# Kernel optimization log

Hardware: AMD Instinct MI355X
Metric: run time of the kernel (lower is better)

## Reference

```python
import jax, jax.numpy as jnp
import numpy as np
from jax import lax

BAD = -10000.0
K = 10
W = 512  # window_size


def setup_inputs() -> dict:
    key = jax.random.key(0)
    k1, k2, k3, k4 = jax.random.split(key, 4)
    S, B, P, D, R = 4, 256, 32768, 256, 1000
    return {
        "relation": jax.random.randint(k1, (S, B), 0, R, dtype=jnp.int32),
        "head": jax.random.randint(k2, (S, B), 0, P, dtype=jnp.int32),
        "entity_embedding": jax.random.normal(k3, (S, P, D), dtype=jnp.float32),
        "relation_embedding": jax.random.normal(k4, (R, D), dtype=jnp.float32),
    }


def reference(relation, head, entity_embedding, relation_embedding):
    S, B = relation.shape
    P, D = entity_embedding.shape[1], entity_embedding.shape[2]
    Q = S * B            # total queries after all_gather
    NBEST = K + 1
    n_rep = -(-P // W)   # ceil

    # all_gather of queries across shards (every shard sees all queries)
    rel_all = relation.reshape(-1)                                   # (Q,)
    head_emb_all = entity_embedding[jnp.arange(S)[:, None], head]    # (S,B,D)
    head_emb_all = head_emb_all.reshape(Q, D)
    # DistMult score_tails: <h, r, t> ; fold h*r into one query vector
    qvec = head_emb_all * relation_embedding[rel_all]                # (Q,D)

    init_sc = jnp.full((S, Q, NBEST), BAD, dtype=jnp.float32)
    init_ix = jnp.full((S, Q, NBEST), P, dtype=jnp.int32)

    def step(carry, w):
        sc, ix = carry
        start = w * W
        # local idx of this window, clamped like the torch mask branch
        raw = start + jnp.arange(W, dtype=jnp.int32)                 # (W,)
        valid = raw < P
        slide = jnp.where(valid, raw, P - 1)
        neg = lax.dynamic_slice_in_dim(entity_embedding,
                                       jnp.minimum(start, P - W), W, axis=1)  # (S,W,D)
        scores_w = jnp.einsum('qd,swd->sqw', qvec, neg)              # (S,Q,W)
        scores_w = scores_w + BAD * (~valid).astype(scores_w.dtype)
        all_sc = jnp.concatenate([scores_w, sc], axis=-1)            # (S,Q,W+NBEST)
        all_ix = jnp.concatenate(
            [jnp.broadcast_to(slide, (S, Q, W)), ix], axis=-1)
        top_sc, top_pos = lax.top_k(all_sc, NBEST)
        top_ix = jnp.take_along_axis(all_ix, top_pos, axis=-1)
        return (top_sc, top_ix), None

    (best_sc, best_ix), _ = lax.scan(step, (init_sc, init_ix),
                                     jnp.arange(n_rep, dtype=jnp.int32))

    # all_to_all: (src_shard, dst_shard, bs, nbest) -> (dst, src, bs, nbest)
    best_sc = best_sc.reshape(S, S, B, NBEST).transpose(1, 0, 2, 3)
    best_ix = best_ix.reshape(S, S, B, NBEST).transpose(1, 0, 2, 3)

    # mask out placeholder / padding local indices (shard_counts == P)
    best_sc = best_sc + BAD * (best_ix >= P).astype(best_sc.dtype)

    # shard_and_idx_to_entity: interleaved global ids, padded column for idx==P
    base = jnp.arange(P, dtype=jnp.int32)[None, :] * S \
        + jnp.arange(S, dtype=jnp.int32)[:, None]                    # (S,P)
    table = jnp.concatenate(
        [base, jnp.full((S, 1), -1, dtype=jnp.int32)], axis=1)       # (S,P+1)
    src = jnp.arange(S, dtype=jnp.int32)[None, :, None, None]
    best_gid = table[src, best_ix]                                   # (S,S,B,NBEST)

    # per destination shard: merge the S per-source-shard top-(k+1) lists
    sc_flat = best_sc.transpose(0, 2, 1, 3).reshape(S, B, S * NBEST)
    gid_flat = best_gid.transpose(0, 2, 1, 3).reshape(S, B, S * NBEST)
    topk_sc, topk_pos = lax.top_k(sc_flat, K)                        # (S,B,K)
    topk_gid = jnp.take_along_axis(gid_flat, topk_pos, axis=-1)
    return topk_gid, topk_sc
```

## Files before the change

### kernel.cpp

```cpp
#include <hip/hip_runtime.h>

#define SS 4
#define BB 256
#define PP 32768
#define DD 256
#define QQ 1024
#define NN 131072
#define KTOP 10
#define QTILE 128
#define WQ 32
#define NCHUNK 64
#define CHROWS 2048
#define PANEL 64
#define NPANEL (CHROWS / PANEL)
#define JCH 8
#define MSLOT 20
#define ROWG 33
#define ROWE (ROWG * 8)
#define PANB (PANEL * ROWG * 16)
#define KEYMASK 0xFFFFF800u
#define MWS 132
#define CVB 4096

typedef __attribute__((ext_vector_type(8))) short bf16x8;
typedef __attribute__((ext_vector_type(4))) short s16x4;
typedef __attribute__((ext_vector_type(4))) float f32x4;
typedef __attribute__((ext_vector_type(16))) float f32x16;
typedef __attribute__((ext_vector_type(4))) unsigned int u32x4;

static __device__ __forceinline__ short f2bf(float f) {
    union { float f; unsigned u; } v; v.f = f;
    unsigned r = (v.u + 0x7FFFu + ((v.u >> 16) & 1u)) >> 16;
    return (short)r;
}
static __device__ __forceinline__ unsigned umax(unsigned a, unsigned b) { return a > b ? a : b; }
static __device__ __forceinline__ unsigned umin(unsigned a, unsigned b) { return a < b ? a : b; }
static __device__ __forceinline__ unsigned med3u(unsigned k, unsigned a, unsigned b) {
    unsigned d;
    asm("v_med3_u32 %0, %1, %2, %3" : "=v"(d) : "v"(k), "v"(a), "v"(b));
    return d;
}

__global__ void prep_kernel(const int* __restrict__ rel, const int* __restrict__ head,
                            const float* __restrict__ E, const float* __restrict__ R,
                            short* __restrict__ Ebf, short* __restrict__ qbf) {
    if (blockIdx.x < CVB) {
        size_t base = (size_t)blockIdx.x * 8192;
        #pragma unroll
        for (int c = 0; c < 8; c++) {
            size_t idx = base + (size_t)c * 1024 + (size_t)threadIdx.x * 4;
            f32x4 a = *(const f32x4*)(E + idx);
            s16x4 o;
            o[0] = f2bf(a[0]); o[1] = f2bf(a[1]); o[2] = f2bf(a[2]); o[3] = f2bf(a[3]);
            *(s16x4*)(Ebf + idx) = o;
        }
    } else {
        int q = blockIdx.x - CVB, d = threadIdx.x;
        int s1 = q >> 8;
        float f = E[((size_t)(s1 * PP + head[q])) * DD + d] * R[(size_t)rel[q] * DD + d];
        qbf[q * DD + d] = f2bf(f);
    }
}

__launch_bounds__(256, 2)
__global__ void score_topk_kernel(const short* __restrict__ Ebf, const short* __restrict__ qbf,
                                  unsigned* __restrict__ parts) {
    __shared__ __align__(16) char smem[2 * PANB];

    const int tid  = threadIdx.x;
    const int wave = tid >> 6;
    const int lane = tid & 63;
    const int lh   = lane >> 5;
    const int ln   = lane & 31;
    const int mtile = blockIdx.x >> 6;
    const int chunk = blockIdx.x & 63;

    short* const buf0 = (short*)smem;
    short* const buf1 = (short*)(smem + PANB);

    bf16x8 afrag[16];
    {
        const int arow = mtile * QTILE + wave * WQ + ln;
        #pragma unroll
        for (int ks = 0; ks < 16; ks++)
            afrag[ks] = *(const bf16x8*)(qbf + arow * DD + ks * 16 + lh * 8);
    }

    unsigned lst[16][4];
    #pragma unroll
    for (int r = 0; r < 16; r++)
        #pragma unroll
        for (int i = 0; i < 4; i++) lst[r][i] = 0u;

    const int n0c = chunk * CHROWS;

    const int srow = tid >> 5, sslot = tid & 31;
    const int goff = srow * DD + sslot * 8;
    const int loff = srow * ROWE + sslot * 8;

    const short* const rb0a = buf0 + ln * ROWE + lh * 8;
    const short* const rb0b = rb0a + 32 * ROWE;
    const short* const rb1a = buf1 + ln * ROWE + lh * 8;
    const short* const rb1b = rb1a + 32 * ROWE;

    bf16x8 st[8];

    {
        const short* pp = Ebf + (size_t)n0c * DD;
        #pragma unroll
        for (int it = 0; it < 8; it++)
            st[it] = *(const bf16x8*)(pp + goff + it * 2048);
        #pragma unroll
        for (int it = 0; it < 8; it++)
            *(bf16x8*)(buf0 + loff + it * (8 * ROWE)) = st[it];
    }

    #define PREFETCH(pnext)                                                        \
        {                                                                          \
            const short* pp = Ebf + (size_t)(n0c + (pnext) * PANEL) * DD;          \
            _Pragma("unroll")                                                      \
            for (int it = 0; it < 8; it++)                                         \
                st[it] = *(const bf16x8*)(pp + goff + it * 2048);                  \
        }
    #define STORE_TO(bufp)                                                         \
        {                                                                          \
            _Pragma("unroll")                                                      \
            for (int it = 0; it < 8; it++)                                         \
                *(bf16x8*)((bufp) + loff + it * (8 * ROWE)) = st[it];              \
        }
    #define COMPUTE(ra, rb, pcur)                                                  \
        {                                                                          \
            f32x16 acc0, acc1;                                                     \
            _Pragma("unroll")                                                      \
            for (int r = 0; r < 16; r++) { acc0[r] = 256.0f; acc1[r] = 256.0f; }   \
            _Pragma("unroll")                                                      \
            for (int ks = 0; ks < 16; ks++) {                                      \
                bf16x8 x0 = *(const bf16x8*)((ra) + ks * 16);                      \
                bf16x8 x1 = *(const bf16x8*)((rb) + ks * 16);                      \
                acc0 = __builtin_amdgcn_mfma_f32_32x32x16_bf16(afrag[ks], x0, acc0, 0, 0, 0); \
                acc1 = __builtin_amdgcn_mfma_f32_32x32x16_bf16(afrag[ks], x1, acc1, 0, 0, 0); \
            }                                                                      \
            const unsigned c0 = (unsigned)((pcur) * 64 + ln);                      \
            const unsigned c1 = c0 + 32u;                                          \
            _Pragma("unroll")                                                      \
            for (int r = 0; r < 16; r++) {                                         \
                unsigned key = (__float_as_uint(acc0[r]) & KEYMASK) | c0;          \
                unsigned n0 = med3u(key, lst[r][0], lst[r][1]);                    \
                unsigned n1 = med3u(key, lst[r][1], lst[r][2]);                    \
                unsigned n2 = med3u(key, lst[r][2], lst[r][3]);                    \
                lst[r][3] = umax(key, lst[r][3]);                                  \
                lst[r][0] = n0; lst[r][1] = n1; lst[r][2] = n2;                    \
            }                                                                      \
            _Pragma("unroll")                                                      \
            for (int r = 0; r < 16; r++) {                                         \
                unsigned key = (__float_as_uint(acc1[r]) & KEYMASK) | c1;          \
                unsigned n0 = med3u(key, lst[r][0], lst[r][1]);                    \
                unsigned n1 = med3u(key, lst[r][1], lst[r][2]);                    \
                unsigned n2 = med3u(key, lst[r][2], lst[r][3]);                    \
                lst[r][3] = umax(key, lst[r][3]);                                  \
                lst[r][0] = n0; lst[r][1] = n1; lst[r][2] = n2;                    \
            }                                                                      \
        }

    for (int p = 0; p < NPANEL; p += 2) {
        __syncthreads();
        PREFETCH(p + 1);
        COMPUTE(rb0a, rb0b, p);
        STORE_TO(buf1);
        __syncthreads();
        if (p + 2 < NPANEL) PREFETCH(p + 2);
        COMPUTE(rb1a, rb1b, p + 1);
        if (p + 2 < NPANEL) STORE_TO(buf0);
    }

    #undef PREFETCH
    #undef STORE_TO
    #undef COMPUTE

    __syncthreads();
    unsigned* mw = (unsigned*)smem + (size_t)wave * (WQ * MWS);
    #pragma unroll
    for (int r = 0; r < 16; r++) {
        int q = (r & 3) + 8 * (r >> 2) + 4 * lh;
        u32x4 v; v[0] = lst[r][0]; v[1] = lst[r][1]; v[2] = lst[r][2]; v[3] = lst[r][3];
        *(u32x4*)(mw + q * MWS + ln * 4) = v;
    }
    if (lane < 32) {
        unsigned rr[JCH];
        #pragma unroll
        for (int i = 0; i < JCH; i++) rr[i] = 0u;
        #pragma unroll
        for (int j = 0; j < 32; j++) {
            u32x4 v = *(const u32x4*)(mw + lane * MWS + j * 4);
            #pragma unroll
            for (int e = 0; e < 4; e++) {
                unsigned x = v[e];
                unsigned t0 = med3u(x, rr[0], rr[1]);
                unsigned t1 = med3u(x, rr[1], rr[2]);
                unsigned t2 = med3u(x, rr[2], rr[3]);
                unsigned t3 = med3u(x, rr[3], rr[4]);
                unsigned t4 = med3u(x, rr[4], rr[5]);
                unsigned t5 = med3u(x, rr[5], rr[6]);
                unsigned t6 = med3u(x, rr[6], rr[7]);
                rr[7] = umax(x, rr[7]);
                rr[0]=t0; rr[1]=t1; rr[2]=t2; rr[3]=t3; rr[4]=t4; rr[5]=t5; rr[6]=t6;
            }
        }
        const int qg = mtile * QTILE + wave * WQ + lane;
        unsigned* dst = parts + ((size_t)qg * NCHUNK + chunk) * JCH;
        #pragma unroll
        for (int i = 0; i < JCH; i++) dst[i] = rr[JCH - 1 - i];
    }
}

__global__ void finalize_kernel(const int* __restrict__ rel, const int* __restrict__ head,
                                const float* __restrict__ E, const float* __restrict__ R,
                                const unsigned* __restrict__ parts, float* __restrict__ out) {
    __shared__ float qv[DD];
    __shared__ int   gl[MSLOT];
    __shared__ float rsc[MSLOT];
    __shared__ int   rgid[MSLOT];

    const int q = blockIdx.x;
    const int tid = threadIdx.x;
    const int wave = tid >> 6, lane = tid & 63;
    const int s1 = q >> 8;

    qv[tid] = E[((size_t)(s1 * PP + head[q])) * DD + tid] * R[(size_t)rel[q] * DD + tid];

    if (wave == 0) {
        unsigned run[JCH];
        const unsigned* src = parts + ((size_t)q * NCHUNK + lane) * JCH;
        #pragma unroll
        for (int j = 0; j < JCH; j++) run[j] = src[j];
        for (int r = 0; r < MSLOT; r++) {
            unsigned best = run[0]; int bl = lane;
            #pragma unroll
            for (int off = 32; off >= 1; off >>= 1) {
                unsigned ob = __shfl_xor(best, off);
                int ol = __shfl_xor(bl, off);
                if (ob > best || (ob == best && ol < bl)) { best = ob; bl = ol; }
            }
            if (lane == bl) {
                int col = (int)(best & 0x7FFu);
                int n = lane * CHROWS + col;
                gl[r] = ((n & (PP - 1)) << 2) | (n >> 15);
                #pragma unroll
                for (int j = 0; j < JCH - 1; j++) run[j] = run[j + 1];
                run[JCH - 1] = 0u;
            }
        }
    }
    __syncthreads();

    f32x4 qq = *(const f32x4*)(qv + lane * 4);
    #pragma unroll
    for (int c = 0; c < MSLOT / 4; c++) {
        int j = wave * (MSLOT / 4) + c;
        int gid = gl[j];
        int n = (gid & 3) * PP + (gid >> 2);
        f32x4 ev = *(const f32x4*)(E + (size_t)n * DD + lane * 4);
        f32x4 p = qq * ev;
        float s = (p[0] + p[1]) + (p[2] + p[3]);
        #pragma unroll
        for (int off = 32; off >= 1; off >>= 1) s += __shfl_xor(s, off);
        if (lane == 0) { rsc[j] = s; rgid[j] = gid; }
    }
    __syncthreads();

    if (tid < 64) {
        float a = (tid < MSLOT) ? rsc[tid] : -1e30f;
        int   g = (tid < MSLOT) ? rgid[tid] : 0;
        for (int r = 0; r < KTOP; r++) {
            float ps = a; int pg = g; int plm = tid;
            #pragma unroll
            for (int off = 32; off >= 1; off >>= 1) {
                float os = __shfl_xor(ps, off);
                int   og = __shfl_xor(pg, off);
                int   ol = __shfl_xor(plm, off);
                if (os > ps || (os == ps && ol < plm)) { ps = os; pg = og; plm = ol; }
            }
            if (tid == 0) {
                out[q * KTOP + r]             = (float)pg;
                out[QQ * KTOP + q * KTOP + r] = ps;
            }
            if (tid == plm) a = -1e30f;
        }
    }
}

extern "C" void kernel_launch(void* const* d_in, const int* in_sizes, int n_in,
                              void* d_out, int out_size, void* d_ws, size_t ws_size,
                              hipStream_t stream) {
    const int*   rel  = (const int*)d_in[0];
    const int*   head = (const int*)d_in[1];
    const float* E    = (const float*)d_in[2];
    const float* R    = (const float*)d_in[3];

    char* ws = (char*)d_ws;
    short* Ebf = (short*)ws;
    short* qbf = (short*)(ws + (size_t)NN * DD * 2);
    unsigned* parts = (unsigned*)(ws + (size_t)NN * DD * 2 + (size_t)QQ * DD * 2);

    prep_kernel<<<dim3(CVB + QQ), dim3(256), 0, stream>>>(rel, head, E, R, Ebf, qbf);
    score_topk_kernel<<<dim3((QQ / QTILE) * NCHUNK), dim3(256), 0, stream>>>(Ebf, qbf, parts);
    finalize_kernel<<<dim3(QQ), dim3(256), 0, stream>>>(rel, head, E, R, parts, (float*)d_out);
}
```

Measured before the change: 307.6 us.

## Stage panels via direct global-to-LDS loads with XOR swizzle and software-pipelined top-k

```diff
diff --git a/kernel.cpp b/kernel.cpp
--- a/kernel.cpp
+++ b/kernel.cpp
@@ -15,11 +15,9 @@
 #define NPANEL (CHROWS / PANEL)
 #define JCH 8
 #define MSLOT 20
-#define ROWG 33
-#define ROWE (ROWG * 8)
-#define PANB (PANEL * ROWG * 16)
+#define PANB (PANEL * DD * 2)
 #define KEYMASK 0xFFFFF800u
-#define MWS 132
+#define MWS 128
 #define CVB 4096
 
 typedef __attribute__((ext_vector_type(8))) short bf16x8;
@@ -34,7 +32,6 @@
     return (short)r;
 }
 static __device__ __forceinline__ unsigned umax(unsigned a, unsigned b) { return a > b ? a : b; }
-static __device__ __forceinline__ unsigned umin(unsigned a, unsigned b) { return a < b ? a : b; }
 static __device__ __forceinline__ unsigned med3u(unsigned k, unsigned a, unsigned b) {
     unsigned d;
     asm("v_med3_u32 %0, %1, %2, %3" : "=v"(d) : "v"(k), "v"(a), "v"(b));
@@ -74,9 +71,7 @@
     const int ln   = lane & 31;
     const int mtile = blockIdx.x >> 6;
     const int chunk = blockIdx.x & 63;
-
-    short* const buf0 = (short*)smem;
-    short* const buf1 = (short*)(smem + PANB);
+    const int wavu = __builtin_amdgcn_readfirstlane(tid) >> 6;
 
     bf16x8 afrag[16];
     {
@@ -92,98 +87,91 @@
         #pragma unroll
         for (int i = 0; i < 4; i++) lst[r][i] = 0u;
 
-    const int n0c = chunk * CHROWS;
-
-    const int srow = tid >> 5, sslot = tid & 31;
-    const int goff = srow * DD + sslot * 8;
-    const int loff = srow * ROWE + sslot * 8;
-
-    const short* const rb0a = buf0 + ln * ROWE + lh * 8;
-    const short* const rb0b = rb0a + 32 * ROWE;
-    const short* const rb1a = buf1 + ln * ROWE + lh * 8;
-    const short* const rb1b = rb1a + 32 * ROWE;
-
-    bf16x8 st[8];
-
-    {
-        const short* pp = Ebf + (size_t)n0c * DD;
-        #pragma unroll
-        for (int it = 0; it < 8; it++)
-            st[it] = *(const bf16x8*)(pp + goff + it * 2048);
-        #pragma unroll
-        for (int it = 0; it < 8; it++)
-            *(bf16x8*)(buf0 + loff + it * (8 * ROWE)) = st[it];
-    }
-
-    #define PREFETCH(pnext)                                                        \
-        {                                                                          \
-            const short* pp = Ebf + (size_t)(n0c + (pnext) * PANEL) * DD;          \
-            _Pragma("unroll")                                                      \
-            for (int it = 0; it < 8; it++)                                         \
-                st[it] = *(const bf16x8*)(pp + goff + it * 2048);                  \
-        }
-    #define STORE_TO(bufp)                                                         \
-        {                                                                          \
-            _Pragma("unroll")                                                      \
-            for (int it = 0; it < 8; it++)                                         \
-                *(bf16x8*)((bufp) + loff + it * (8 * ROWE)) = st[it];              \
-        }
-    #define COMPUTE(ra, rb, pcur)                                                  \
-        {                                                                          \
-            f32x16 acc0, acc1;                                                     \
-            _Pragma("unroll")                                                      \
-            for (int r = 0; r < 16; r++) { acc0[r] = 256.0f; acc1[r] = 256.0f; }   \
-            _Pragma("unroll")                                                      \
-            for (int ks = 0; ks < 16; ks++) {                                      \
-                bf16x8 x0 = *(const bf16x8*)((ra) + ks * 16);                      \
-                bf16x8 x1 = *(const bf16x8*)((rb) + ks * 16);                      \
-                acc0 = __builtin_amdgcn_mfma_f32_32x32x16_bf16(afrag[ks], x0, acc0, 0, 0, 0); \
-                acc1 = __builtin_amdgcn_mfma_f32_32x32x16_bf16(afrag[ks], x1, acc1, 0, 0, 0); \
-            }                                                                      \
-            const unsigned c0 = (unsigned)((pcur) * 64 + ln);                      \
-            const unsigned c1 = c0 + 32u;                                          \
-            _Pragma("unroll")                                                      \
-            for (int r = 0; r < 16; r++) {                                         \
-                unsigned key = (__float_as_uint(acc0[r]) & KEYMASK) | c0;          \
-                unsigned n0 = med3u(key, lst[r][0], lst[r][1]);                    \
-                unsigned n1 = med3u(key, lst[r][1], lst[r][2]);                    \
-                unsigned n2 = med3u(key, lst[r][2], lst[r][3]);                    \
-                lst[r][3] = umax(key, lst[r][3]);                                  \
-                lst[r][0] = n0; lst[r][1] = n1; lst[r][2] = n2;                    \
-            }                                                                      \
-            _Pragma("unroll")                                                      \
-            for (int r = 0; r < 16; r++) {                                         \
-                unsigned key = (__float_as_uint(acc1[r]) & KEYMASK) | c1;          \
-                unsigned n0 = med3u(key, lst[r][0], lst[r][1]);                    \
-                unsigned n1 = med3u(key, lst[r][1], lst[r][2]);                    \
-                unsigned n2 = med3u(key, lst[r][2], lst[r][3]);                    \
-                lst[r][3] = umax(key, lst[r][3]);                                  \
-                lst[r][0] = n0; lst[r][1] = n1; lst[r][2] = n2;                    \
-            }                                                                      \
-        }
+    int addrk[16];
+    #pragma unroll
+    for (int ks = 0; ks < 16; ks++)
+        addrk[ks] = ln * 512 + ((((ks << 1) | lh) ^ (ln & 7)) << 4);
+
+    int soff[8];
+    #pragma unroll
+    for (int it = 0; it < 8; it++) {
+        int row = (((wavu * 8 + it) << 1) | lh);
+        soff[it] = row * 512 + ((ln ^ (row & 7)) << 4);
+    }
+
+    const char* const pb = (const char*)(Ebf + (size_t)(chunk * CHROWS) * DD);
+
+    #define STAGE(POFF, LOFF)                                                          \
+        {                                                                              \
+            _Pragma("unroll")                                                          \
+            for (int it = 0; it < 8; it++)                                             \
+                __builtin_amdgcn_global_load_lds(                                      \
+                    (const __attribute__((address_space(1))) void*)(pb + (POFF) + soff[it]), \
+                    (__attribute__((address_space(3))) void*)(smem + (LOFF) + (wavu * 8 + it) * 1024), \
+                    16, 0, 0);                                                         \
+        }
+
+    #define MFMA_PANEL(A0, A1, LOFF)                                                   \
+        {                                                                              \
+            _Pragma("unroll")                                                          \
+            for (int r = 0; r < 16; r++) { A0[r] = 256.0f; A1[r] = 256.0f; }           \
+            _Pragma("unroll")                                                          \
+            for (int ks = 0; ks < 16; ks++) {                                          \
+                bf16x8 x0 = *(const bf16x8*)(smem + addrk[ks] + (LOFF));               \
+                bf16x8 x1 = *(const bf16x8*)(smem + addrk[ks] + (LOFF) + 16384);       \
+                A0 = __builtin_amdgcn_mfma_f32_32x32x16_bf16(afrag[ks], x0, A0, 0, 0, 0); \
+                A1 = __builtin_amdgcn_mfma_f32_32x32x16_bf16(afrag[ks], x1, A1, 0, 0, 0); \
+            }                                                                          \
+        }
+
+    #define KEYS(A0, A1, PIDX)                                                         \
+        {                                                                              \
+            const unsigned c0k = (unsigned)((PIDX) * 64 + ln);                         \
+            const unsigned c1k = c0k + 32u;                                            \
+            _Pragma("unroll")                                                          \
+            for (int r = 0; r < 16; r++) {                                             \
+                unsigned key = (__float_as_uint(A0[r]) & KEYMASK) | c0k;               \
+                unsigned n0 = med3u(key, lst[r][0], lst[r][1]);                        \
+                unsigned n1 = med3u(key, lst[r][1], lst[r][2]);                        \
+                unsigned n2 = med3u(key, lst[r][2], lst[r][3]);                        \
+                lst[r][3] = umax(key, lst[r][3]);                                      \
+                lst[r][0] = n0; lst[r][1] = n1; lst[r][2] = n2;                        \
+                key = (__float_as_uint(A1[r]) & KEYMASK) | c1k;                        \
+                n0 = med3u(key, lst[r][0], lst[r][1]);                                 \
+                n1 = med3u(key, lst[r][1], lst[r][2]);                                 \
+                n2 = med3u(key, lst[r][2], lst[r][3]);                                 \
+                lst[r][3] = umax(key, lst[r][3]);                                      \
+                lst[r][0] = n0; lst[r][1] = n1; lst[r][2] = n2;                        \
+            }                                                                          \
+        }
+
+    f32x16 accA0, accA1, accB0, accB1;
+
+    STAGE(0, 0);
+    __syncthreads();
 
     for (int p = 0; p < NPANEL; p += 2) {
+        STAGE((p + 1) * PANB, PANB);
+        MFMA_PANEL(accA0, accA1, 0);
+        if (p > 0) KEYS(accB0, accB1, p - 1);
         __syncthreads();
-        PREFETCH(p + 1);
-        COMPUTE(rb0a, rb0b, p);
-        STORE_TO(buf1);
+        if (p + 2 < NPANEL) STAGE((p + 2) * PANB, 0);
+        MFMA_PANEL(accB0, accB1, PANB);
+        KEYS(accA0, accA1, p);
         __syncthreads();
-        if (p + 2 < NPANEL) PREFETCH(p + 2);
-        COMPUTE(rb1a, rb1b, p + 1);
-        if (p + 2 < NPANEL) STORE_TO(buf0);
-    }
-
-    #undef PREFETCH
-    #undef STORE_TO
-    #undef COMPUTE
-
-    __syncthreads();
+    }
+    KEYS(accB0, accB1, NPANEL - 1);
+
+    #undef STAGE
+    #undef MFMA_PANEL
+    #undef KEYS
+
     unsigned* mw = (unsigned*)smem + (size_t)wave * (WQ * MWS);
     #pragma unroll
     for (int r = 0; r < 16; r++) {
         int q = (r & 3) + 8 * (r >> 2) + 4 * lh;
         u32x4 v; v[0] = lst[r][0]; v[1] = lst[r][1]; v[2] = lst[r][2]; v[3] = lst[r][3];
-        *(u32x4*)(mw + q * MWS + ln * 4) = v;
+        *(u32x4*)(mw + q * MWS + ((ln * 4) ^ ((q & 7) << 2))) = v;
     }
     if (lane < 32) {
         unsigned rr[JCH];
@@ -191,7 +179,7 @@
         for (int i = 0; i < JCH; i++) rr[i] = 0u;
         #pragma unroll
         for (int j = 0; j < 32; j++) {
-            u32x4 v = *(const u32x4*)(mw + lane * MWS + j * 4);
+            u32x4 v = *(const u32x4*)(mw + lane * MWS + ((j * 4) ^ ((lane & 7) << 2)));
             #pragma unroll
             for (int e = 0; e < 4; e++) {
                 unsigned x = v[e];
```

New measurement: 330.9 us. +7.6%, slower.
